# Optimization experiments

Hardware: AMD Instinct MI355X
Metric: run time of the kernel (lower is better)

## Reference

```python
import jax, jax.numpy as jnp
import numpy as np

B, S, H, D, E = 4, 2048, 16, 64, 1024
BASE_SCALE = 0.03125  # config.base_scale = 1/sqrt(n_embed)
SQK_INIT_VAL = 1.0


def setup_inputs() -> dict:
    key = jax.random.key(0)
    ks = jax.random.split(key, 5)
    x = jax.random.normal(ks[0], (B, S, E), dtype=jnp.float32)
    Wq = jax.random.normal(ks[1], (E, E), dtype=jnp.float32) * 0.02
    Wk = jax.random.normal(ks[2], (E, E), dtype=jnp.float32) * 0.02
    Wv = jax.random.normal(ks[3], (E, E), dtype=jnp.float32) * 0.02
    sqk = BASE_SCALE * jnp.ones((E,), dtype=jnp.float32)
    # RoPE frequencies: theta = 10000^(-2i/D), angles[s, i] = s * theta_i
    theta = 1.0 / (10000.0 ** (np.arange(0, D, 2, dtype=np.float32) / D))  # [D/2]
    angles = np.arange(S, dtype=np.float32)[:, None] * theta[None, :]       # [S, D/2]
    freqs_cos = jnp.asarray(np.cos(angles), dtype=jnp.float32)
    freqs_sin = jnp.asarray(np.sin(angles), dtype=jnp.float32)
    return {"x": x, "Wq": Wq, "Wk": Wk, "Wv": Wv, "sqk": sqk,
            "freqs_cos": freqs_cos, "freqs_sin": freqs_sin}


def _rope(t, cos, sin):
    # t: [B, S, H, D]; cos/sin: [S, D/2] broadcast as [1, S, 1, D/2]
    tr = t.reshape(*t.shape[:-1], D // 2, 2)
    a, b = tr[..., 0], tr[..., 1]
    c = cos[None, :, None, :]
    s = sin[None, :, None, :]
    out = jnp.stack([a * c - b * s, a * s + b * c], axis=-1)
    return out.reshape(t.shape)


def _l2norm(t):
    return t / jnp.linalg.norm(t, axis=-1, keepdims=True)


def reference(x, Wq, Wk, Wv, sqk, freqs_cos, freqs_sin):
    # Linear (torch: x @ W.T), no bias
    q = jnp.einsum('bse,oe->bso', x, Wq).reshape(B, S, H, D)
    k = jnp.einsum('bse,oe->bso', x, Wk).reshape(B, S, H, D)
    v = jnp.einsum('bse,oe->bso', x, Wv).reshape(B, S, H, D)
    q = _rope(q, freqs_cos, freqs_sin)
    k = _rope(k, freqs_cos, freqs_sin)
    # -> [B, H, S, D]
    q = q.transpose(0, 2, 1, 3)
    k = k.transpose(0, 2, 1, 3)
    v = v.transpose(0, 2, 1, 3)
    scale = (sqk * (SQK_INIT_VAL / BASE_SCALE)).reshape(1, H, 1, D)
    q = scale * _l2norm(q)
    k = scale * _l2norm(k)
    scores = jnp.einsum('bhqd,bhkd->bhqk', q, k) * (D ** -0.5)
    attn = jax.nn.softmax(scores, axis=-1)
    out = jnp.einsum('bhqk,bhkd->bhqd', attn, v)  # [B, H, S, D]
    return out.transpose(0, 2, 1, 3).reshape(B, S, E)
```

## Files before the change

kernel.cpp:

```cpp
#include <hip/hip_runtime.h>
#include <stdint.h>

#define B_ 4
#define S_ 2048
#define H_ 16
#define D_ 64
#define E_ 1024

typedef __bf16 bf16x8 __attribute__((ext_vector_type(8)));
typedef float f32x4 __attribute__((ext_vector_type(4)));
typedef unsigned short u16x4 __attribute__((ext_vector_type(4)));

static __device__ __forceinline__ unsigned short f2bf(float f) {
    unsigned u = __builtin_bit_cast(unsigned, f);
    u += 0x7fffu + ((u >> 16) & 1u);
    return (unsigned short)(u >> 16);
}

static __device__ __forceinline__ f32x4 mfma16(bf16x8 a, bf16x8 b, f32x4 c) {
    return __builtin_amdgcn_mfma_f32_16x16x32_bf16(a, b, c, 0, 0, 0);
}

static __device__ __forceinline__ void gload_lds16(const void* g, void* l) {
    __builtin_amdgcn_global_load_lds(
        (__attribute__((address_space(1))) void*)g,
        (__attribute__((address_space(3))) void*)l, 16, 0, 0);
}

__global__ void cvt_f32_bf16_k(const float* __restrict__ src,
                               unsigned short* __restrict__ dst, int n4) {
    int stride = gridDim.x * blockDim.x;
    for (int i = blockIdx.x * blockDim.x + threadIdx.x; i < n4; i += stride) {
        float4 v = reinterpret_cast<const float4*>(src)[i];
        u16x4 o;
        o[0] = f2bf(v.x); o[1] = f2bf(v.y); o[2] = f2bf(v.z); o[3] = f2bf(v.w);
        reinterpret_cast<u16x4*>(dst)[i] = o;
    }
}

__global__ __launch_bounds__(256) void qkv_gemm_k(
    const unsigned short* __restrict__ xbf,
    const unsigned short* __restrict__ wbf,
    const float* __restrict__ sqk,
    const float* __restrict__ fcos,
    const float* __restrict__ fsin,
    unsigned short* __restrict__ qws,
    unsigned short* __restrict__ kws,
    unsigned short* __restrict__ vtws)
{
    __shared__ unsigned short As[128 * 32];
    __shared__ unsigned short Bs[128 * 32];
    const int tid = threadIdx.x;
    const int w = tid >> 6, lane = tid & 63;
    const int wr = w >> 1, wc = w & 1;
    const int mbase = blockIdx.y * 128;
    const int nbase = blockIdx.x * 128;
    const int c15 = lane & 15;
    const int g4 = lane >> 4;
    const int kb8 = g4 * 8;

    const f32x4 zero4 = {0.f, 0.f, 0.f, 0.f};
    f32x4 acc[4][4];
#pragma unroll
    for (int m = 0; m < 4; m++)
#pragma unroll
        for (int n = 0; n < 4; n++) acc[m][n] = zero4;

    for (int kt = 0; kt < 32; ++kt) {
        const int k0 = kt * 32;
#pragma unroll
        for (int i = 0; i < 2; i++) {
            int g = (i * 4 + w) * 64 + lane;
            int row = g >> 2, slot = g & 3;
            gload_lds16(xbf + (size_t)(mbase + row) * E_ + k0 + slot * 8,
                        As + (i * 4 + w) * 512);
            gload_lds16(wbf + (size_t)(nbase + row) * E_ + k0 + slot * 8,
                        Bs + (i * 4 + w) * 512);
        }
        asm volatile("s_waitcnt vmcnt(0)" ::: "memory");
        __syncthreads();
        bf16x8 af[4], bfr[4];
#pragma unroll
        for (int m = 0; m < 4; m++)
            af[m] = *(const bf16x8*)(As + (wr * 64 + m * 16 + c15) * 32 + kb8);
#pragma unroll
        for (int n = 0; n < 4; n++)
            bfr[n] = *(const bf16x8*)(Bs + (wc * 64 + n * 16 + c15) * 32 + kb8);
#pragma unroll
        for (int m = 0; m < 4; m++)
#pragma unroll
            for (int n = 0; n < 4; n++)
                acc[m][n] = mfma16(af[m], bfr[n], acc[m][n]);
        __syncthreads();
    }

    const int gcb = nbase + wc * 64;
    const int qkv = gcb >> 10;
    const int oo = gcb & 1023;
    const int h = oo >> 6;

    if (qkv < 2) {
        unsigned short* dst = (qkv == 0) ? qws : kws;
        const float qs = (qkv == 0) ? 0.125f : 1.0f;
        float cs4[4];
#pragma unroll
        for (int n = 0; n < 4; n++)
            cs4[n] = sqk[oo + n * 16 + c15] * 32.0f * qs;
#pragma unroll
        for (int m = 0; m < 4; m++) {
#pragma unroll
            for (int r = 0; r < 4; r++) {
                const int grow = mbase + wr * 64 + m * 16 + g4 * 4 + r;
                const int bb = grow >> 11;
                const int srow = grow & 2047;
                float nv[4], ss = 0.f;
#pragma unroll
                for (int n = 0; n < 4; n++) {
                    const int d = n * 16 + c15;
                    const float a = acc[m][n][r];
                    const float other = __shfl_xor(a, 1);
                    const float cc = fcos[srow * 32 + (d >> 1)];
                    const float sn = fsin[srow * 32 + (d >> 1)];
                    const float rv = (d & 1) ? (other * sn + a * cc) : (a * cc - other * sn);
                    nv[n] = rv;
                    ss += rv * rv;
                }
#pragma unroll
                for (int mask = 1; mask < 16; mask <<= 1)
                    ss += __shfl_xor(ss, mask);
                const float rn = rsqrtf(ss);
                unsigned short* rp = dst + ((size_t)(bb * H_ + h) * S_ + srow) * D_;
#pragma unroll
                for (int n = 0; n < 4; n++)
                    rp[n * 16 + c15] = f2bf(nv[n] * rn * cs4[n]);
            }
        }
    } else {
#pragma unroll
        for (int m = 0; m < 4; m++) {
            const int grow0 = mbase + wr * 64 + m * 16 + g4 * 4;
            const int bb = grow0 >> 11;
            const int srow0 = grow0 & 2047;
#pragma unroll
            for (int n = 0; n < 4; n++) {
                const int d = n * 16 + c15;
                u16x4 pk;
#pragma unroll
                for (int r = 0; r < 4; r++) pk[r] = f2bf(acc[m][n][r]);
                *reinterpret_cast<u16x4*>(vtws + ((size_t)(bb * H_ + h) * D_ + d) * S_ + srow0) = pk;
            }
        }
    }
}

__global__ __launch_bounds__(256) void attn_fwd_k(
    const unsigned short* __restrict__ qws,
    const unsigned short* __restrict__ kws,
    const unsigned short* __restrict__ vtws,
    float* __restrict__ out)
{
    __shared__ unsigned short Klds[64 * 64];
    __shared__ unsigned short Vlds[64 * 64];
    __shared__ unsigned short Plds[64 * 72];
    const int tid = threadIdx.x;
    const int w = tid >> 6, lane = tid & 63;
    const int c15 = lane & 15;
    const int g4 = lane >> 4;
    const int kb8 = g4 * 8;
    const int bh = blockIdx.y;
    const int b = bh >> 4, h = bh & 15;
    const int q0 = blockIdx.x * 64;

    bf16x8 qf[2];
    {
        const unsigned short* qp =
            qws + ((size_t)bh * S_ + (q0 + w * 16 + c15)) * D_ + kb8;
        qf[0] = *(const bf16x8*)qp;
        qf[1] = *(const bf16x8*)(qp + 32);
    }

    const f32x4 zero4 = {0.f, 0.f, 0.f, 0.f};
    float mrow[4], lrow[4];
    f32x4 o[4];
#pragma unroll
    for (int n = 0; n < 4; n++) o[n] = zero4;
#pragma unroll
    for (int r = 0; r < 4; r++) { mrow[r] = -3.0e38f; lrow[r] = 0.f; }

    const char* kbase_g = (const char*)(kws + (size_t)bh * S_ * D_);
    const unsigned short* vbase_g = vtws + (size_t)bh * D_ * S_;

    for (int kt = 0; kt < 32; ++kt) {
#pragma unroll
        for (int i = 0; i < 2; i++) {
            int loff = ((i * 4 + w) * 64 + lane) * 16;
            int soff = loff ^ (((loff >> 7) & 7) << 4);
            gload_lds16(kbase_g + (size_t)kt * 8192 + soff,
                        (char*)Klds + (i * 4 + w) * 1024);
        }
#pragma unroll
        for (int i = 0; i < 2; i++) {
            int g = (i * 4 + w) * 64 + lane;
            int row = g >> 3, slot = g & 7;
            int soff = (slot * 16) ^ ((row & 7) << 4);
            gload_lds16((const char*)(vbase_g + (size_t)row * S_ + kt * 64) + soff,
                        (char*)Vlds + (i * 4 + w) * 1024);
        }
        asm volatile("s_waitcnt vmcnt(0)" ::: "memory");
        __syncthreads();

        f32x4 sf[4];
#pragma unroll
        for (int n = 0; n < 4; n++) {
            sf[n] = zero4;
            const int kvc = n * 16 + c15;
            const char* kro = (const char*)Klds + kvc * 128;
            const int sw = (kvc & 7) << 4;
            sf[n] = mfma16(qf[0], *(const bf16x8*)(kro + ((kb8 * 2) ^ sw)), sf[n]);
            sf[n] = mfma16(qf[1], *(const bf16x8*)(kro + ((kb8 * 2 + 64) ^ sw)), sf[n]);
        }

        float mn[4];
#pragma unroll
        for (int r = 0; r < 4; r++)
            mn[r] = fmaxf(fmaxf(sf[0][r], sf[1][r]), fmaxf(sf[2][r], sf[3][r]));
#pragma unroll
        for (int mask = 1; mask < 16; mask <<= 1)
#pragma unroll
            for (int r = 0; r < 4; r++)
                mn[r] = fmaxf(mn[r], __shfl_xor(mn[r], mask));
        float alpha[4];
#pragma unroll
        for (int r = 0; r < 4; r++) {
            float mt = fmaxf(mrow[r], mn[r]);
            alpha[r] = __expf(mrow[r] - mt);
            mrow[r] = mt;
        }
        float rs[4] = {0.f, 0.f, 0.f, 0.f};
#pragma unroll
        for (int n = 0; n < 4; n++)
#pragma unroll
            for (int r = 0; r < 4; r++) {
                float p = __expf(sf[n][r] - mrow[r]);
                sf[n][r] = p;
                rs[r] += p;
            }
#pragma unroll
        for (int mask = 1; mask < 16; mask <<= 1)
#pragma unroll
            for (int r = 0; r < 4; r++)
                rs[r] += __shfl_xor(rs[r], mask);
#pragma unroll
        for (int r = 0; r < 4; r++)
            lrow[r] = lrow[r] * alpha[r] + rs[r];
#pragma unroll
        for (int n = 0; n < 4; n++)
#pragma unroll
            for (int r = 0; r < 4; r++)
                o[n][r] *= alpha[r];

        {
            const int pr0 = w * 16 + g4 * 4;
#pragma unroll
            for (int n = 0; n < 4; n++) {
                const int pc = n * 16 + c15;
#pragma unroll
                for (int r = 0; r < 4; r++)
                    Plds[(pr0 + r) * 72 + pc] = f2bf(sf[n][r]);
            }
        }
        asm volatile("s_waitcnt lgkmcnt(0)" ::: "memory");

        bf16x8 pf[2];
        {
            const unsigned short* pp = Plds + (w * 16 + c15) * 72 + kb8;
            pf[0] = *(const bf16x8*)pp;
            pf[1] = *(const bf16x8*)(pp + 32);
        }
#pragma unroll
        for (int n = 0; n < 4; n++) {
            const int dc = n * 16 + c15;
            const char* vro = (const char*)Vlds + dc * 128;
            const int sw = (dc & 7) << 4;
            o[n] = mfma16(pf[0], *(const bf16x8*)(vro + ((kb8 * 2) ^ sw)), o[n]);
            o[n] = mfma16(pf[1], *(const bf16x8*)(vro + ((kb8 * 2 + 64) ^ sw)), o[n]);
        }
        __syncthreads();
    }

    const int so0 = q0 + w * 16 + g4 * 4;
#pragma unroll
    for (int r = 0; r < 4; r++) {
        const float inv = 1.0f / lrow[r];
        float* op = out + ((size_t)b * S_ + so0 + r) * E_ + h * D_;
#pragma unroll
        for (int n = 0; n < 4; n++)
            op[n * 16 + c15] = o[n][r] * inv;
    }
}

extern "C" void kernel_launch(void* const* d_in, const int* in_sizes, int n_in,
                              void* d_out, int out_size, void* d_ws, size_t ws_size,
                              hipStream_t stream) {
    (void)in_sizes; (void)n_in; (void)out_size; (void)ws_size;
    const float* x = (const float*)d_in[0];
    const float* Wq = (const float*)d_in[1];
    const float* Wk = (const float*)d_in[2];
    const float* Wv = (const float*)d_in[3];
    const float* sqk = (const float*)d_in[4];
    const float* fcos = (const float*)d_in[5];
    const float* fsin = (const float*)d_in[6];

    char* ws = (char*)d_ws;
    size_t off = 0;
    unsigned short* xbf = (unsigned short*)(ws + off); off += (size_t)B_ * S_ * E_ * 2;
    unsigned short* wbf = (unsigned short*)(ws + off); off += (size_t)3 * E_ * E_ * 2;
    unsigned short* qws = (unsigned short*)(ws + off); off += (size_t)B_ * H_ * S_ * D_ * 2;
    unsigned short* kws = (unsigned short*)(ws + off); off += (size_t)B_ * H_ * S_ * D_ * 2;
    unsigned short* vtws = (unsigned short*)(ws + off); off += (size_t)B_ * H_ * S_ * D_ * 2;

    cvt_f32_bf16_k<<<dim3(2048), dim3(256), 0, stream>>>(x, xbf, (B_ * S_ * E_) / 4);
    cvt_f32_bf16_k<<<dim3(512), dim3(256), 0, stream>>>(Wq, wbf, (E_ * E_) / 4);
    cvt_f32_bf16_k<<<dim3(512), dim3(256), 0, stream>>>(Wk, wbf + E_ * E_, (E_ * E_) / 4);
    cvt_f32_bf16_k<<<dim3(512), dim3(256), 0, stream>>>(Wv, wbf + 2 * E_ * E_, (E_ * E_) / 4);

    qkv_gemm_k<<<dim3(24, 64), dim3(256), 0, stream>>>(xbf, wbf, sqk, fcos, fsin,
                                                       qws, kws, vtws);
    attn_fwd_k<<<dim3(32, 64), dim3(256), 0, stream>>>(qws, kws, vtws, (float*)d_out);
}
```

Measured before the change: 392.0 us.

## Double-buffer attention K/V tiles, use exp2 softmax with lazy rescale, XCD-aware block mapping

The attention kernel now double-buffers K/V tiles in LDS, so the next tile's global-to-LDS load overlaps compute on the current one and one barrier per iteration goes away. Softmax folds log2(e) into the Q scale and calls v_exp_f32 directly. It skips the max/rescale shuffles unless a row max rises by more than 8, and it defers the row-sum reduction to the end. It also packs P to bf16 with v_cvt_pk_bf16_f32, remaps blocks so heads cluster per XCD for L2 reuse, and adds s_setprio around MFMA blocks in both kernels. In exchange it uses more LDS and relies on the bounded unnormalized exponent staying in fp32 range.

```diff
diff --git a/kernel.cpp b/kernel.cpp
--- a/kernel.cpp
+++ b/kernel.cpp
@@ -15,6 +15,18 @@
     unsigned u = __builtin_bit_cast(unsigned, f);
     u += 0x7fffu + ((u >> 16) & 1u);
     return (unsigned short)(u >> 16);
+}
+
+static __device__ __forceinline__ float fexp2(float x) {
+    float r;
+    asm("v_exp_f32 %0, %1" : "=v"(r) : "v"(x));
+    return r;
+}
+
+static __device__ __forceinline__ unsigned cvtpk_bf16(float lo, float hi) {
+    unsigned r;
+    asm("v_cvt_pk_bf16_f32 %0, %1, %2" : "=v"(r) : "v"(lo), "v"(hi));
+    return r;
 }
 
 static __device__ __forceinline__ f32x4 mfma16(bf16x8 a, bf16x8 b, f32x4 c) {
@@ -86,11 +98,13 @@
 #pragma unroll
         for (int n = 0; n < 4; n++)
             bfr[n] = *(const bf16x8*)(Bs + (wc * 64 + n * 16 + c15) * 32 + kb8);
+        __builtin_amdgcn_s_setprio(1);
 #pragma unroll
         for (int m = 0; m < 4; m++)
 #pragma unroll
             for (int n = 0; n < 4; n++)
                 acc[m][n] = mfma16(af[m], bfr[n], acc[m][n]);
+        __builtin_amdgcn_s_setprio(0);
         __syncthreads();
     }
 
@@ -101,7 +115,7 @@
 
     if (qkv < 2) {
         unsigned short* dst = (qkv == 0) ? qws : kws;
-        const float qs = (qkv == 0) ? 0.125f : 1.0f;
+        const float qs = (qkv == 0) ? (0.125f * 1.44269504f) : 1.0f;
         float cs4[4];
 #pragma unroll
         for (int n = 0; n < 4; n++)
@@ -159,17 +173,20 @@
     const unsigned short* __restrict__ vtws,
     float* __restrict__ out)
 {
-    __shared__ unsigned short Klds[64 * 64];
-    __shared__ unsigned short Vlds[64 * 64];
-    __shared__ unsigned short Plds[64 * 72];
+    __shared__ unsigned short Klds[2 * 64 * 64];
+    __shared__ unsigned short Vlds[2 * 64 * 64];
+    __shared__ unsigned short Plds[64 * 68];
     const int tid = threadIdx.x;
     const int w = tid >> 6, lane = tid & 63;
     const int c15 = lane & 15;
     const int g4 = lane >> 4;
     const int kb8 = g4 * 8;
-    const int bh = blockIdx.y;
+
+    const int id = blockIdx.x;
+    const int xcd = id & 7, c = id >> 3;
+    const int bh = xcd * 8 + (c >> 5);
+    const int q0 = (c & 31) * 64;
     const int b = bh >> 4, h = bh & 15;
-    const int q0 = blockIdx.x * 64;
 
     bf16x8 qf[2];
     {
@@ -190,103 +207,134 @@
     const char* kbase_g = (const char*)(kws + (size_t)bh * S_ * D_);
     const unsigned short* vbase_g = vtws + (size_t)bh * D_ * S_;
 
-    for (int kt = 0; kt < 32; ++kt) {
+    auto STAGE = [&](int t, int bsel) {
 #pragma unroll
         for (int i = 0; i < 2; i++) {
             int loff = ((i * 4 + w) * 64 + lane) * 16;
             int soff = loff ^ (((loff >> 7) & 7) << 4);
-            gload_lds16(kbase_g + (size_t)kt * 8192 + soff,
-                        (char*)Klds + (i * 4 + w) * 1024);
+            gload_lds16(kbase_g + (size_t)t * 8192 + soff,
+                        (char*)Klds + bsel * 8192 + (i * 4 + w) * 1024);
         }
 #pragma unroll
         for (int i = 0; i < 2; i++) {
             int g = (i * 4 + w) * 64 + lane;
             int row = g >> 3, slot = g & 7;
             int soff = (slot * 16) ^ ((row & 7) << 4);
-            gload_lds16((const char*)(vbase_g + (size_t)row * S_ + kt * 64) + soff,
-                        (char*)Vlds + (i * 4 + w) * 1024);
-        }
-        asm volatile("s_waitcnt vmcnt(0)" ::: "memory");
-        __syncthreads();
+            gload_lds16((const char*)(vbase_g + (size_t)row * S_ + t * 64) + soff,
+                        (char*)Vlds + bsel * 8192 + (i * 4 + w) * 1024);
+        }
+    };
+
+    STAGE(0, 0);
+    asm volatile("s_waitcnt vmcnt(0)" ::: "memory");
+    __syncthreads();
+
+    int cur = 0;
+    for (int kt = 0; kt < 32; ++kt) {
+        if (kt + 1 < 32) STAGE(kt + 1, cur ^ 1);
+
+        const char* kb_l = (const char*)Klds + cur * 8192;
+        const char* vb_l = (const char*)Vlds + cur * 8192;
 
         f32x4 sf[4];
+        bf16x8 kf[4][2];
+#pragma unroll
+        for (int n = 0; n < 4; n++) {
+            const int kvc = n * 16 + c15;
+            const char* kro = kb_l + kvc * 128;
+            const int sw = (kvc & 7) << 4;
+            kf[n][0] = *(const bf16x8*)(kro + ((kb8 * 2) ^ sw));
+            kf[n][1] = *(const bf16x8*)(kro + ((kb8 * 2 + 64) ^ sw));
+        }
+        __builtin_amdgcn_s_setprio(1);
 #pragma unroll
         for (int n = 0; n < 4; n++) {
             sf[n] = zero4;
-            const int kvc = n * 16 + c15;
-            const char* kro = (const char*)Klds + kvc * 128;
-            const int sw = (kvc & 7) << 4;
-            sf[n] = mfma16(qf[0], *(const bf16x8*)(kro + ((kb8 * 2) ^ sw)), sf[n]);
-            sf[n] = mfma16(qf[1], *(const bf16x8*)(kro + ((kb8 * 2 + 64) ^ sw)), sf[n]);
-        }
-
-        float mn[4];
+            sf[n] = mfma16(qf[0], kf[n][0], sf[n]);
+            sf[n] = mfma16(qf[1], kf[n][1], sf[n]);
+        }
+        __builtin_amdgcn_s_setprio(0);
+
+        float pmax[4];
 #pragma unroll
         for (int r = 0; r < 4; r++)
-            mn[r] = fmaxf(fmaxf(sf[0][r], sf[1][r]), fmaxf(sf[2][r], sf[3][r]));
-#pragma unroll
-        for (int mask = 1; mask < 16; mask <<= 1)
+            pmax[r] = fmaxf(fmaxf(sf[0][r], sf[1][r]), fmaxf(sf[2][r], sf[3][r]));
+        int ok = (pmax[0] <= mrow[0] + 8.0f) & (pmax[1] <= mrow[1] + 8.0f) &
+                 (pmax[2] <= mrow[2] + 8.0f) & (pmax[3] <= mrow[3] + 8.0f);
+        if (!__all(ok)) {
+#pragma unroll
+            for (int r = 0; r < 4; r++) {
+                float mn = pmax[r];
+#pragma unroll
+                for (int mask = 1; mask < 16; mask <<= 1)
+                    mn = fmaxf(mn, __shfl_xor(mn, mask));
+                float mt = fmaxf(mrow[r], mn);
+                float al = fexp2(mrow[r] - mt);
+                mrow[r] = mt;
+                lrow[r] *= al;
+#pragma unroll
+                for (int n = 0; n < 4; n++) o[n][r] *= al;
+            }
+        }
+#pragma unroll
+        for (int n = 0; n < 4; n++)
 #pragma unroll
             for (int r = 0; r < 4; r++)
-                mn[r] = fmaxf(mn[r], __shfl_xor(mn[r], mask));
-        float alpha[4];
-#pragma unroll
-        for (int r = 0; r < 4; r++) {
-            float mt = fmaxf(mrow[r], mn[r]);
-            alpha[r] = __expf(mrow[r] - mt);
-            mrow[r] = mt;
-        }
-        float rs[4] = {0.f, 0.f, 0.f, 0.f};
-#pragma unroll
-        for (int n = 0; n < 4; n++)
-#pragma unroll
-            for (int r = 0; r < 4; r++) {
-                float p = __expf(sf[n][r] - mrow[r]);
-                sf[n][r] = p;
-                rs[r] += p;
-            }
-#pragma unroll
-        for (int mask = 1; mask < 16; mask <<= 1)
-#pragma unroll
-            for (int r = 0; r < 4; r++)
-                rs[r] += __shfl_xor(rs[r], mask);
+                sf[n][r] = fexp2(sf[n][r] - mrow[r]);
 #pragma unroll
         for (int r = 0; r < 4; r++)
-            lrow[r] = lrow[r] * alpha[r] + rs[r];
-#pragma unroll
-        for (int n = 0; n < 4; n++)
-#pragma unroll
-            for (int r = 0; r < 4; r++)
-                o[n][r] *= alpha[r];
+            lrow[r] += (sf[0][r] + sf[1][r]) + (sf[2][r] + sf[3][r]);
 
         {
             const int pr0 = w * 16 + g4 * 4;
 #pragma unroll
-            for (int n = 0; n < 4; n++) {
-                const int pc = n * 16 + c15;
-#pragma unroll
-                for (int r = 0; r < 4; r++)
-                    Plds[(pr0 + r) * 72 + pc] = f2bf(sf[n][r]);
+            for (int r = 0; r < 4; r++) {
+                unsigned w01 = cvtpk_bf16(sf[0][r], sf[1][r]);
+                unsigned w23 = cvtpk_bf16(sf[2][r], sf[3][r]);
+                unsigned short* row = Plds + (pr0 + r) * 68;
+                row[c15] = (unsigned short)w01;
+                row[16 + c15] = (unsigned short)(w01 >> 16);
+                row[32 + c15] = (unsigned short)w23;
+                row[48 + c15] = (unsigned short)(w23 >> 16);
             }
         }
         asm volatile("s_waitcnt lgkmcnt(0)" ::: "memory");
 
         bf16x8 pf[2];
         {
-            const unsigned short* pp = Plds + (w * 16 + c15) * 72 + kb8;
+            const unsigned short* pp = Plds + (w * 16 + c15) * 68 + kb8;
             pf[0] = *(const bf16x8*)pp;
             pf[1] = *(const bf16x8*)(pp + 32);
         }
+        bf16x8 vf[4][2];
 #pragma unroll
         for (int n = 0; n < 4; n++) {
             const int dc = n * 16 + c15;
-            const char* vro = (const char*)Vlds + dc * 128;
+            const char* vro = vb_l + dc * 128;
             const int sw = (dc & 7) << 4;
-            o[n] = mfma16(pf[0], *(const bf16x8*)(vro + ((kb8 * 2) ^ sw)), o[n]);
-            o[n] = mfma16(pf[1], *(const bf16x8*)(vro + ((kb8 * 2 + 64) ^ sw)), o[n]);
-        }
-        __syncthreads();
-    }
+            vf[n][0] = *(const bf16x8*)(vro + ((kb8 * 2) ^ sw));
+            vf[n][1] = *(const bf16x8*)(vro + ((kb8 * 2 + 64) ^ sw));
+        }
+        __builtin_amdgcn_s_setprio(1);
+#pragma unroll
+        for (int n = 0; n < 4; n++) {
+            o[n] = mfma16(pf[0], vf[n][0], o[n]);
+            o[n] = mfma16(pf[1], vf[n][1], o[n]);
+        }
+        __builtin_amdgcn_s_setprio(0);
+
+        if (kt + 1 < 32) {
+            asm volatile("s_waitcnt vmcnt(0)" ::: "memory");
+            __syncthreads();
+            cur ^= 1;
+        }
+    }
+
+#pragma unroll
+    for (int mask = 1; mask < 16; mask <<= 1)
+#pragma unroll
+        for (int r = 0; r < 4; r++)
+            lrow[r] += __shfl_xor(lrow[r], mask);
 
     const int so0 = q0 + w * 16 + g4 * 4;
 #pragma unroll
@@ -326,5 +374,5 @@
 
     qkv_gemm_k<<<dim3(24, 64), dim3(256), 0, stream>>>(xbf, wbf, sqk, fcos, fsin,
                                                        qws, kws, vtws);
-    attn_fwd_k<<<dim3(32, 64), dim3(256), 0, stream>>>(qws, kws, vtws, (float*)d_out);
-}
+    attn_fwd_k<<<dim3(2048), dim3(256), 0, stream>>>(qws, kws, vtws, (float*)d_out);
+}
```

Result: faster. 356.2 us (-9.1%).
